# Optimization experiments

Hardware: AMD Instinct MI355X
Metric: run time of the kernel (lower is better)

## Reference

```python
import jax, jax.numpy as jnp
import numpy as np

B, C, H, W = 16, 512, 64, 64
G = 32
CG = C // G       # per-group channels = 16


def setup_inputs() -> dict:
    key = jax.random.key(0)
    ks = jax.random.split(key, 6)
    def w(k, shape, fan_in):
        return (jax.random.normal(k, shape, jnp.float32) / np.float32(np.sqrt(fan_in)))
    return {
        "x": jax.random.normal(ks[0], (B, C, H, W), jnp.float32),
        "conv1_w": w(ks[1], (CG, CG), CG), "conv1_b": jnp.zeros((CG,), jnp.float32),
        "convh_w": w(ks[2], (CG, CG), CG), "convh_b": jnp.zeros((CG,), jnp.float32),
        "convw_w": w(ks[3], (CG, CG), CG), "convw_b": jnp.zeros((CG,), jnp.float32),
        "conv3_w": w(ks[4], (CG, CG, 3, 3), CG * 9), "conv3_b": jnp.zeros((CG,), jnp.float32),
        "gn_w": jnp.ones((CG,), jnp.float32), "gn_b": jnp.zeros((CG,), jnp.float32),
    }


def _conv1x1(y, w, b):
    # y: [N, Ci, L]  w: [Co, Ci]  -> [N, Co, L]
    return jnp.einsum('oi,bil->bol', w, y) + b[None, :, None]


def _ema_forward(x, conv1_w, conv1_b, convh_w, convh_b, convw_w, convw_b,
                 conv3_w, conv3_b, gn_w, gn_b):
    b, c, h, w = x.shape
    g, cg, hw = G, CG, h * w
    bg = b * g
    xg = x.reshape(bg, cg, h, w)

    # coordinate pooling: row means [bg,cg,h], col means [bg,cg,w]
    x_h = xg.mean(axis=3)                     # [bg, cg, h]
    x_w = xg.mean(axis=2)                     # [bg, cg, w]
    y = jnp.concatenate([x_h, x_w], axis=2)   # [bg, cg, h+w]
    y = jax.nn.relu(_conv1x1(y, conv1_w, conv1_b))
    y_h, y_w = y[:, :, :h], y[:, :, h:]

    a_h = jax.nn.sigmoid(_conv1x1(y_h, convh_w, convh_b))[:, :, :, None]  # [bg,cg,h,1]
    a_w = jax.nn.sigmoid(_conv1x1(y_w, convw_w, convw_b))[:, :, None, :]  # [bg,cg,1,w]

    x1 = xg * a_h * a_w

    # GroupNorm(num_groups=1): normalize over (cg,h,w) per sample, affine per channel
    mu = x1.mean(axis=(1, 2, 3), keepdims=True)
    var = ((x1 - mu) ** 2).mean(axis=(1, 2, 3), keepdims=True)
    x2 = (x1 - mu) * jax.lax.rsqrt(var + 1e-5)
    x2 = x2 * gn_w[None, :, None, None] + gn_b[None, :, None, None]

    # 3x3 conv branch
    x3 = jax.lax.conv_general_dilated(
        xg, conv3_w, window_strides=(1, 1), padding='SAME',
        dimension_numbers=('NCHW', 'OIHW', 'NCHW'))
    x3 = jax.nn.relu(x3 + conv3_b[None, :, None, None])

    A2 = jax.nn.softmax(x2.reshape(bg, cg, hw), axis=-1)  # [bg,cg,hw]
    A3 = jax.nn.softmax(x3.reshape(bg, cg, hw), axis=-1)
    V2 = x2.mean(axis=(2, 3))                              # [bg,cg]
    V3 = x3.mean(axis=(2, 3))

    s2 = jnp.einsum('bc,bcl->bl', V2, A3)  # [bg, hw]
    s3 = jnp.einsum('bc,bcl->bl', V3, A2)
    s = jax.nn.softmax(s2 + s3, axis=-1).reshape(bg, 1, h, w)

    return (xg * s).reshape(b, c, h, w)


def reference(x, conv1_w, conv1_b, convh_w, convh_b, convw_w, convw_b,
              conv3_w, conv3_b, gn_w, gn_b):
    return _ema_forward(x, conv1_w, conv1_b, convh_w, convh_b, convw_w, convw_b,
                        conv3_w, conv3_b, gn_w, gn_b)
```

## Files before the change

### kernel.cpp

```cpp
#include <hip/hip_runtime.h>
#include <hip/hip_bf16.h>

#define CHW  65536
#define CHW4 16384

__device__ __forceinline__ float wred(float v){
#pragma unroll
  for (int o = 32; o; o >>= 1) v += __shfl_xor(v, o, 64);
  return v;
}
__device__ __forceinline__ float wred16(float v){
#pragma unroll
  for (int o = 8; o; o >>= 1) v += __shfl_xor(v, o, 64);
  return v;
}
__device__ __forceinline__ float bf2f(unsigned short u){
  return __uint_as_float(((unsigned)u) << 16);
}

__global__ __launch_bounds__(1024) void k1_attn(const float* __restrict__ x,
    const float* __restrict__ w1, const float* __restrict__ b1,
    const float* __restrict__ wh, const float* __restrict__ bh,
    const float* __restrict__ ww, const float* __restrict__ bw,
    float* __restrict__ aH, float* __restrict__ aW)
{
  __shared__ float rs[1024];
  __shared__ float cs[1024];
  __shared__ float ym[2048];
  int tid = threadIdx.x, bg = blockIdx.x;
  const float4* x4 = (const float4*)x + (size_t)bg * CHW4;
  cs[tid] = 0.f;
  __syncthreads();
  int h = tid >> 4, lane = tid & 63;
#pragma unroll 4
  for (int k = 0; k < 16; ++k){
    float4 v = x4[k*1024 + tid];
    float s = v.x + v.y + v.z + v.w;
    s = wred16(s);
    if ((tid & 15) == 0) rs[k*64 + h] = s;
    v.x += __shfl_xor(v.x, 16); v.x += __shfl_xor(v.x, 32);
    v.y += __shfl_xor(v.y, 16); v.y += __shfl_xor(v.y, 32);
    v.z += __shfl_xor(v.z, 16); v.z += __shfl_xor(v.z, 32);
    v.w += __shfl_xor(v.w, 16); v.w += __shfl_xor(v.w, 32);
    if (lane < 16){
      atomicAdd(&cs[k*64 + lane*4 + 0], v.x);
      atomicAdd(&cs[k*64 + lane*4 + 1], v.y);
      atomicAdd(&cs[k*64 + lane*4 + 2], v.z);
      atomicAdd(&cs[k*64 + lane*4 + 3], v.w);
    }
  }
  __syncthreads();
  for (int ol = tid; ol < 2048; ol += 1024){
    int o = ol >> 7, l = ol & 127;
    float acc = b1[o];
#pragma unroll
    for (int i = 0; i < 16; ++i){
      float mv = (l < 64 ? rs[i*64 + l] : cs[i*64 + (l-64)]) * (1.f/64.f);
      acc = fmaf(w1[o*16 + i], mv, acc);
    }
    ym[o*128 + l] = fmaxf(acc, 0.f);
  }
  __syncthreads();
  for (int ol = tid; ol < 2048; ol += 1024){
    int q = ol >> 10;
    int o = (ol >> 6) & 15;
    int p = ol & 63;
    const float* Wm = q ? ww : wh;
    float acc = q ? bw[o] : bh[o];
#pragma unroll
    for (int i = 0; i < 16; ++i)
      acc = fmaf(Wm[o*16 + i], ym[i*128 + q*64 + p], acc);
    float sg = 1.f / (1.f + __expf(-acc));
    (q ? aW : aH)[((size_t)bg*16 + o)*64 + p] = sg;
  }
}

__global__ __launch_bounds__(1024) void k2_stats(const float* __restrict__ x,
    const float* __restrict__ aH, const float* __restrict__ aW,
    const float* __restrict__ gnw, const float* __restrict__ gnb,
    float* __restrict__ MU, float* __restrict__ RSTD,
    float* __restrict__ V2, float* __restrict__ Z2)
{
  __shared__ __align__(16) float ahs[1024], aws[1024];
  __shared__ float chpart[256], zpart[256];
  __shared__ float red1[16], red2[16];
  __shared__ float murs[2], sc_s[16], of_s[16];
  int tid = threadIdx.x, bg = blockIdx.x;
  const float4* x4 = (const float4*)x + (size_t)bg * CHW4;
  ahs[tid] = aH[(size_t)bg*1024 + tid];
  aws[tid] = aW[(size_t)bg*1024 + tid];
  __syncthreads();
  int h = tid >> 4, w4 = tid & 15, lane = tid & 63, wv = tid >> 6;
  const float4* aws4 = (const float4*)aws;
  float s1 = 0.f, s2 = 0.f;
#pragma unroll 4
  for (int k = 0; k < 16; ++k){
    float4 v = x4[k*1024 + tid];
    float ah = ahs[k*64 + h];
    float4 aw = aws4[k*16 + w4];
    float4 x1;
    x1.x = v.x * ah * aw.x;
    x1.y = v.y * ah * aw.y;
    x1.z = v.z * ah * aw.z;
    x1.w = v.w * ah * aw.w;
    float csum = x1.x + x1.y + x1.z + x1.w;
    s1 += csum;
    s2 = fmaf(x1.x, x1.x, s2); s2 = fmaf(x1.y, x1.y, s2);
    s2 = fmaf(x1.z, x1.z, s2); s2 = fmaf(x1.w, x1.w, s2);
    float cw = wred(csum);
    if (lane == 0) chpart[k*16 + wv] = cw;
  }
  float r1 = wred(s1), r2 = wred(s2);
  if (lane == 0){ red1[wv] = r1; red2[wv] = r2; }
  __syncthreads();
  if (tid == 0){
    float S = 0.f, SS = 0.f;
#pragma unroll
    for (int i = 0; i < 16; ++i){ S += red1[i]; SS += red2[i]; }
    float mu = S * (1.f/65536.f);
    float var = SS * (1.f/65536.f) - mu*mu;
    float rstd = rsqrtf(var + 1e-5f);
    murs[0] = mu; murs[1] = rstd;
    MU[bg] = mu; RSTD[bg] = rstd;
  }
  __syncthreads();
  if (tid < 16){
    float ch = 0.f;
#pragma unroll
    for (int m = 0; m < 16; ++m) ch += chpart[tid*16 + m];
    float mu = murs[0], rstd = murs[1];
    float g = gnw[tid], b = gnb[tid];
    float sc = rstd * g;
    sc_s[tid] = sc; of_s[tid] = b - mu*sc;
    V2[(size_t)bg*16 + tid] = (ch * (1.f/4096.f) - mu) * sc + b;
  }
  __syncthreads();
#pragma unroll 2
  for (int k = 0; k < 16; ++k){
    float4 v = x4[k*1024 + tid];
    float ah = ahs[k*64 + h];
    float4 aw = aws4[k*16 + w4];
    float sc = sc_s[k], of = of_s[k];
    float z =  __expf(fmaf(v.x * ah * aw.x, sc, of));
    z += __expf(fmaf(v.y * ah * aw.y, sc, of));
    z += __expf(fmaf(v.z * ah * aw.z, sc, of));
    z += __expf(fmaf(v.w * ah * aw.w, sc, of));
    float zw = wred(z);
    if (lane == 0) zpart[k*16 + wv] = zw;
  }
  __syncthreads();
  if (tid < 16){
    float z = 0.f;
#pragma unroll
    for (int m = 0; m < 16; ++m) z += zpart[tid*16 + m];
    Z2[(size_t)bg*16 + tid] = z;
  }
}

#define STR 84
__global__ __launch_bounds__(256, 3) void k3_conv(const float* __restrict__ x,
    const float* __restrict__ w3, const float* __restrict__ b3,
    __hip_bfloat16* __restrict__ X3, float* __restrict__ V3, float* __restrict__ Z3)
{
  __shared__ __align__(16) float in_s[16*10*STR];
  int tid = threadIdx.x;
  int s   = blockIdx.x;
  int bg  = blockIdx.y;
  size_t base  = (size_t)bg * CHW;
  const float4* x4 = (const float4*)x + (size_t)bg * CHW4;
  int lane = tid & 63;
  int cog = __builtin_amdgcn_readfirstlane(tid >> 6);
  int co0 = cog * 4;
  int r  = lane >> 3;
  int w0 = (lane & 7) * 8;
  for (int idx = tid; idx < 2880; idx += 256){
    int q  = idx % 18;
    int rr = (idx / 18) % 10;
    int ci = idx / 180;
    int hh = s*8 - 1 + rr;
    float4 v = make_float4(0.f, 0.f, 0.f, 0.f);
    if (q >= 1 && q <= 16 && (unsigned)hh < 64u)
      v = x4[ci*1024 + hh*16 + (q-1)];
    *(float4*)&in_s[(ci*10 + rr)*STR + q*4] = v;
  }
  float bias[4];
#pragma unroll
  for (int i = 0; i < 4; ++i) bias[i] = b3[co0+i];
  float acc[4][8];
#pragma unroll
  for (int i = 0; i < 4; ++i)
#pragma unroll
    for (int px = 0; px < 8; ++px) acc[i][px] = 0.f;
  __syncthreads();
#pragma unroll 1
  for (int ci = 0; ci < 16; ++ci){
    float wgt[4][9];
#pragma unroll
    for (int i = 0; i < 4; ++i)
#pragma unroll
      for (int t = 0; t < 9; ++t)
        wgt[i][t] = w3[((co0+i)*16 + ci)*9 + t];
#pragma unroll
    for (int dy = 0; dy < 3; ++dy){
      const float* row = &in_s[(ci*10 + r + dy)*STR + w0];
      float4 A0 = *(const float4*)(row);
      float4 A1 = *(const float4*)(row+4);
      float4 A2v = *(const float4*)(row+8);
      float4 A3v = *(const float4*)(row+12);
      float v[16] = {A0.x,A0.y,A0.z,A0.w, A1.x,A1.y,A1.z,A1.w,
                     A2v.x,A2v.y,A2v.z,A2v.w, A3v.x,A3v.y,A3v.z,A3v.w};
#pragma unroll
      for (int dx = 0; dx < 3; ++dx){
#pragma unroll
        for (int px = 0; px < 8; ++px){
          float iv = v[px + dx + 3];
#pragma unroll
          for (int i = 0; i < 4; ++i)
            acc[i][px] = fmaf(wgt[i][dy*3+dx], iv, acc[i][px]);
        }
      }
    }
  }
  int hh = s*8 + r;
  float v3acc[4], z3acc[4];
#pragma unroll
  for (int i = 0; i < 4; ++i){
    union { __hip_bfloat16 hb[8]; uint4 u; } pk;
    v3acc[i] = 0.f; z3acc[i] = 0.f;
#pragma unroll
    for (int px = 0; px < 8; ++px){
      float val = fmaxf(acc[i][px] + bias[i], 0.f);
      __hip_bfloat16 hv = __float2bfloat16(val);
      float vq = __bfloat162float(hv);
      v3acc[i] += vq;
      z3acc[i] += __expf(vq);
      pk.hb[px] = hv;
    }
    *(uint4*)&X3[base + (size_t)(co0+i)*4096 + hh*64 + w0] = pk.u;
  }
#pragma unroll
  for (int i = 0; i < 4; ++i){
    float rv = wred(v3acc[i]);
    float rz = wred(z3acc[i]);
    if (lane == 0){
      atomicAdd(&V3[(size_t)bg*16 + co0 + i], rv);
      atomicAdd(&Z3[(size_t)bg*16 + co0 + i], rz);
    }
  }
}

__global__ __launch_bounds__(1024) void k4_final(const float* __restrict__ x,
    const __hip_bfloat16* __restrict__ X3,
    const float* __restrict__ aH, const float* __restrict__ aW,
    const float* __restrict__ gnw, const float* __restrict__ gnb,
    const float* __restrict__ MU, const float* __restrict__ RSTD,
    const float* __restrict__ V2, const float* __restrict__ Z2,
    const float* __restrict__ V3, const float* __restrict__ Z3,
    float* __restrict__ out)
{
  __shared__ __align__(16) float ahs[1024], aws[1024];
  __shared__ float sc_s[16], of_s[16], p2s[16], p3s[16], red[16];
  __shared__ float invS_s;
  int tid = threadIdx.x, bg = blockIdx.x;
  const float4* x4 = (const float4*)x + (size_t)bg * CHW4;
  const ushort4* X34 = (const ushort4*)X3 + (size_t)bg * CHW4;
  float4* o4 = (float4*)out + (size_t)bg * CHW4;
  ahs[tid] = aH[(size_t)bg*1024 + tid];
  aws[tid] = aW[(size_t)bg*1024 + tid];
  if (tid < 16){
    float mu = MU[bg], rstd = RSTD[bg];
    float g = gnw[tid], b = gnb[tid];
    float sc = rstd*g;
    sc_s[tid] = sc; of_s[tid] = b - mu*sc;
    p2s[tid] = V3[(size_t)bg*16+tid] * (1.f/4096.f) / Z2[(size_t)bg*16+tid];
    p3s[tid] = V2[(size_t)bg*16+tid] / Z3[(size_t)bg*16+tid];
  }
  __syncthreads();
  int h = tid >> 4, w4 = tid & 15, lane = tid & 63, wv = tid >> 6;
  const float4* aws4 = (const float4*)aws;
  float4 tacc = make_float4(0.f,0.f,0.f,0.f);
#pragma unroll 2
  for (int k = 0; k < 16; ++k){
    float4 v = x4[k*1024 + tid];
    ushort4 xu = X34[k*1024 + tid];
    float ah = ahs[k*64 + h];
    float4 aw = aws4[k*16 + w4];
    float sc = sc_s[k], of = of_s[k], p2 = p2s[k], p3 = p3s[k];
    tacc.x += __expf(fmaf(v.x*ah*aw.x, sc, of))*p2 + __expf(bf2f(xu.x))*p3;
    tacc.y += __expf(fmaf(v.y*ah*aw.y, sc, of))*p2 + __expf(bf2f(xu.y))*p3;
    tacc.z += __expf(fmaf(v.z*ah*aw.z, sc, of))*p2 + __expf(bf2f(xu.z))*p3;
    tacc.w += __expf(fmaf(v.w*ah*aw.w, sc, of))*p2 + __expf(bf2f(xu.w))*p3;
  }
  float4 e;
  e.x = __expf(tacc.x); e.y = __expf(tacc.y);
  e.z = __expf(tacc.z); e.w = __expf(tacc.w);
  float es = e.x + e.y + e.z + e.w;
  float r = wred(es);
  if (lane == 0) red[wv] = r;
  __syncthreads();
  if (tid == 0){
    float S = 0.f;
#pragma unroll
    for (int i = 0; i < 16; ++i) S += red[i];
    invS_s = 1.f / S;
  }
  __syncthreads();
  float iS = invS_s;
  float4 ei = make_float4(e.x*iS, e.y*iS, e.z*iS, e.w*iS);
#pragma unroll 4
  for (int k = 0; k < 16; ++k){
    float4 v = x4[k*1024 + tid];
    float4 ov;
    ov.x = v.x * ei.x; ov.y = v.y * ei.y;
    ov.z = v.z * ei.z; ov.w = v.w * ei.w;
    o4[k*1024 + tid] = ov;
  }
}

extern "C" void kernel_launch(void* const* d_in, const int* in_sizes, int n_in,
                              void* d_out, int out_size, void* d_ws, size_t ws_size,
                              hipStream_t stream)
{
  const float* x   = (const float*)d_in[0];
  const float* w1  = (const float*)d_in[1];
  const float* b1  = (const float*)d_in[2];
  const float* wh  = (const float*)d_in[3];
  const float* bh  = (const float*)d_in[4];
  const float* ww  = (const float*)d_in[5];
  const float* bw  = (const float*)d_in[6];
  const float* w3  = (const float*)d_in[7];
  const float* b3  = (const float*)d_in[8];
  const float* gnw = (const float*)d_in[9];
  const float* gnb = (const float*)d_in[10];
  float* out = (float*)d_out;

  float* Wp   = (float*)d_ws;
  float* aH   = Wp;
  float* aW_  = aH + 524288;
  float* MU   = aW_ + 524288;
  float* RSTD = MU + 512;
  float* V2   = RSTD + 512;
  float* Z2   = V2 + 8192;
  float* V3   = Z2 + 8192;
  float* Z3   = V3 + 8192;
  __hip_bfloat16* X3 = (__hip_bfloat16*)(Z3 + 8192);
  (void)ws_size; (void)n_in; (void)in_sizes; (void)out_size;

  hipMemsetAsync(V3, 0, 2 * 8192 * sizeof(float), stream);
  k1_attn <<<512, 1024, 0, stream>>>(x, w1, b1, wh, bh, ww, bw, aH, aW_);
  k3_conv <<<dim3(8, 512), 256, 0, stream>>>(x, w3, b3, X3, V3, Z3);
  k2_stats<<<512, 1024, 0, stream>>>(x, aH, aW_, gnw, gnb, MU, RSTD, V2, Z2);
  k4_final<<<512, 1024, 0, stream>>>(x, X3, aH, aW_, gnw, gnb, MU, RSTD, V2, Z2, V3, Z3, out);
}
```

Before: 512.6 us.

## Fuse attention, stats and final kernels into one megakernel; store exp of conv output

The attention, GroupNorm-stats and final softmax kernels are merged into a single per-group kernel that keeps the H/W attention vectors and statistics in shared memory instead of round-tripping through global memory. The conv kernel now stages input in two 8-channel halves to halve shared memory and raise occupancy. It stores exp(x3) in bf16 so the final pass skips one exp per element, and it writes per-strip partial sums instead of using atomics, which removes the memset. The risks are that the megakernel does three sequential passes over x within one block with heavy LDS use, and that bf16 rounding of exp values changes precision slightly.

```diff
diff --git a/kernel.cpp b/kernel.cpp
--- a/kernel.cpp
+++ b/kernel.cpp
@@ -18,26 +18,131 @@
   return __uint_as_float(((unsigned)u) << 16);
 }
 
-__global__ __launch_bounds__(1024) void k1_attn(const float* __restrict__ x,
+#define STR 84
+__global__ __launch_bounds__(256, 6) void k3_conv(const float* __restrict__ x,
+    const float* __restrict__ w3, const float* __restrict__ b3,
+    __hip_bfloat16* __restrict__ E3,
+    float* __restrict__ V3part, float* __restrict__ Z3part)
+{
+  __shared__ __align__(16) float in_s[8*10*STR];
+  int tid = threadIdx.x;
+  int s   = blockIdx.x;
+  int bg  = blockIdx.y;
+  size_t base  = (size_t)bg * CHW;
+  const float4* x4 = (const float4*)x + (size_t)bg * CHW4;
+  int lane = tid & 63;
+  int cog = __builtin_amdgcn_readfirstlane(tid >> 6);
+  int co0 = cog * 4;
+  int r  = lane >> 3;
+  int w0 = (lane & 7) * 8;
+  float acc[4][8];
+#pragma unroll
+  for (int i = 0; i < 4; ++i)
+#pragma unroll
+    for (int px = 0; px < 8; ++px) acc[i][px] = 0.f;
+
+#pragma unroll 1
+  for (int half = 0; half < 2; ++half){
+    __syncthreads();
+    for (int idx = tid; idx < 1440; idx += 256){
+      int q   = idx % 18;
+      int rr  = (idx / 18) % 10;
+      int ci8 = idx / 180;
+      int hh  = s*8 - 1 + rr;
+      float4 v = make_float4(0.f, 0.f, 0.f, 0.f);
+      if (q >= 1 && q <= 16 && (unsigned)hh < 64u)
+        v = x4[(half*8 + ci8)*1024 + hh*16 + (q-1)];
+      *(float4*)&in_s[(ci8*10 + rr)*STR + q*4] = v;
+    }
+    __syncthreads();
+#pragma unroll 1
+    for (int ci8 = 0; ci8 < 8; ++ci8){
+      int ci = half*8 + ci8;
+      float wgt[4][9];
+#pragma unroll
+      for (int i = 0; i < 4; ++i)
+#pragma unroll
+        for (int t = 0; t < 9; ++t)
+          wgt[i][t] = w3[((co0+i)*16 + ci)*9 + t];
+#pragma unroll
+      for (int dy = 0; dy < 3; ++dy){
+        const float* row = &in_s[(ci8*10 + r + dy)*STR + w0];
+        float4 A0 = *(const float4*)(row);
+        float4 A1 = *(const float4*)(row+4);
+        float4 A2v = *(const float4*)(row+8);
+        float4 A3v = *(const float4*)(row+12);
+        float v[16] = {A0.x,A0.y,A0.z,A0.w, A1.x,A1.y,A1.z,A1.w,
+                       A2v.x,A2v.y,A2v.z,A2v.w, A3v.x,A3v.y,A3v.z,A3v.w};
+#pragma unroll
+        for (int dx = 0; dx < 3; ++dx){
+#pragma unroll
+          for (int px = 0; px < 8; ++px){
+            float iv = v[px + dx + 3];
+#pragma unroll
+            for (int i = 0; i < 4; ++i)
+              acc[i][px] = fmaf(wgt[i][dy*3+dx], iv, acc[i][px]);
+          }
+        }
+      }
+    }
+  }
+  int hh = s*8 + r;
+#pragma unroll
+  for (int i = 0; i < 4; ++i){
+    float bias = b3[co0+i];
+    union { __hip_bfloat16 hb[8]; uint4 u; } pk;
+    float v3acc = 0.f, z3acc = 0.f;
+#pragma unroll
+    for (int px = 0; px < 8; ++px){
+      float val = fmaxf(acc[i][px] + bias, 0.f);
+      float e = __expf(val);
+      v3acc += val;
+      z3acc += e;
+      pk.hb[px] = __float2bfloat16(e);
+    }
+    *(uint4*)&E3[base + (size_t)(co0+i)*4096 + hh*64 + w0] = pk.u;
+    float rv = wred(v3acc);
+    float rz = wred(z3acc);
+    if (lane == 0){
+      V3part[((size_t)bg*8 + s)*16 + co0 + i] = rv;
+      Z3part[((size_t)bg*8 + s)*16 + co0 + i] = rz;
+    }
+  }
+}
+
+__global__ __launch_bounds__(1024, 8) void mega(const float* __restrict__ x,
     const float* __restrict__ w1, const float* __restrict__ b1,
     const float* __restrict__ wh, const float* __restrict__ bh,
     const float* __restrict__ ww, const float* __restrict__ bw,
-    float* __restrict__ aH, float* __restrict__ aW)
+    const float* __restrict__ gnw, const float* __restrict__ gnb,
+    const float* __restrict__ V3part, const float* __restrict__ Z3part,
+    const __hip_bfloat16* __restrict__ E3,
+    float* __restrict__ out)
 {
   __shared__ float rs[1024];
   __shared__ float cs[1024];
   __shared__ float ym[2048];
+  __shared__ __align__(16) float ahs[1024], aws[1024];
+  __shared__ float chpart[256], zpart[256];
+  __shared__ float red1[16], red2[16];
+  __shared__ float murs[2];
+  __shared__ float sc_s[16], of_s[16], v2_s[16], p2s[16], p3s[16];
+  __shared__ float invS_s;
+
   int tid = threadIdx.x, bg = blockIdx.x;
   const float4* x4 = (const float4*)x + (size_t)bg * CHW4;
+  const ushort4* E34 = (const ushort4*)E3 + (size_t)bg * CHW4;
+  float4* o4 = (float4*)out + (size_t)bg * CHW4;
+  int h = tid >> 4, w4 = tid & 15, lane = tid & 63, wv = tid >> 6;
+
   cs[tid] = 0.f;
   __syncthreads();
-  int h = tid >> 4, lane = tid & 63;
 #pragma unroll 4
   for (int k = 0; k < 16; ++k){
     float4 v = x4[k*1024 + tid];
-    float s = v.x + v.y + v.z + v.w;
-    s = wred16(s);
-    if ((tid & 15) == 0) rs[k*64 + h] = s;
+    float srow = v.x + v.y + v.z + v.w;
+    srow = wred16(srow);
+    if ((tid & 15) == 0) rs[k*64 + h] = srow;
     v.x += __shfl_xor(v.x, 16); v.x += __shfl_xor(v.x, 32);
     v.y += __shfl_xor(v.y, 16); v.y += __shfl_xor(v.y, 32);
     v.z += __shfl_xor(v.z, 16); v.z += __shfl_xor(v.z, 32);
@@ -71,26 +176,10 @@
     for (int i = 0; i < 16; ++i)
       acc = fmaf(Wm[o*16 + i], ym[i*128 + q*64 + p], acc);
     float sg = 1.f / (1.f + __expf(-acc));
-    (q ? aW : aH)[((size_t)bg*16 + o)*64 + p] = sg;
-  }
-}
-
-__global__ __launch_bounds__(1024) void k2_stats(const float* __restrict__ x,
-    const float* __restrict__ aH, const float* __restrict__ aW,
-    const float* __restrict__ gnw, const float* __restrict__ gnb,
-    float* __restrict__ MU, float* __restrict__ RSTD,
-    float* __restrict__ V2, float* __restrict__ Z2)
-{
-  __shared__ __align__(16) float ahs[1024], aws[1024];
-  __shared__ float chpart[256], zpart[256];
-  __shared__ float red1[16], red2[16];
-  __shared__ float murs[2], sc_s[16], of_s[16];
-  int tid = threadIdx.x, bg = blockIdx.x;
-  const float4* x4 = (const float4*)x + (size_t)bg * CHW4;
-  ahs[tid] = aH[(size_t)bg*1024 + tid];
-  aws[tid] = aW[(size_t)bg*1024 + tid];
-  __syncthreads();
-  int h = tid >> 4, w4 = tid & 15, lane = tid & 63, wv = tid >> 6;
+    (q ? aws : ahs)[o*64 + p] = sg;
+  }
+  __syncthreads();
+
   const float4* aws4 = (const float4*)aws;
   float s1 = 0.f, s2 = 0.f;
 #pragma unroll 4
@@ -119,9 +208,7 @@
     for (int i = 0; i < 16; ++i){ S += red1[i]; SS += red2[i]; }
     float mu = S * (1.f/65536.f);
     float var = SS * (1.f/65536.f) - mu*mu;
-    float rstd = rsqrtf(var + 1e-5f);
-    murs[0] = mu; murs[1] = rstd;
-    MU[bg] = mu; RSTD[bg] = rstd;
+    murs[0] = mu; murs[1] = rsqrtf(var + 1e-5f);
   }
   __syncthreads();
   if (tid < 16){
@@ -132,9 +219,10 @@
     float g = gnw[tid], b = gnb[tid];
     float sc = rstd * g;
     sc_s[tid] = sc; of_s[tid] = b - mu*sc;
-    V2[(size_t)bg*16 + tid] = (ch * (1.f/4096.f) - mu) * sc + b;
-  }
-  __syncthreads();
+    v2_s[tid] = (ch * (1.f/4096.f) - mu) * sc + b;
+  }
+  __syncthreads();
+
 #pragma unroll 2
   for (int k = 0; k < 16; ++k){
     float4 v = x4[k*1024 + tid];
@@ -150,163 +238,50 @@
   }
   __syncthreads();
   if (tid < 16){
-    float z = 0.f;
-#pragma unroll
-    for (int m = 0; m < 16; ++m) z += zpart[tid*16 + m];
-    Z2[(size_t)bg*16 + tid] = z;
-  }
-}
-
-#define STR 84
-__global__ __launch_bounds__(256, 3) void k3_conv(const float* __restrict__ x,
-    const float* __restrict__ w3, const float* __restrict__ b3,
-    __hip_bfloat16* __restrict__ X3, float* __restrict__ V3, float* __restrict__ Z3)
-{
-  __shared__ __align__(16) float in_s[16*10*STR];
-  int tid = threadIdx.x;
-  int s   = blockIdx.x;
-  int bg  = blockIdx.y;
-  size_t base  = (size_t)bg * CHW;
-  const float4* x4 = (const float4*)x + (size_t)bg * CHW4;
-  int lane = tid & 63;
-  int cog = __builtin_amdgcn_readfirstlane(tid >> 6);
-  int co0 = cog * 4;
-  int r  = lane >> 3;
-  int w0 = (lane & 7) * 8;
-  for (int idx = tid; idx < 2880; idx += 256){
-    int q  = idx % 18;
-    int rr = (idx / 18) % 10;
-    int ci = idx / 180;
-    int hh = s*8 - 1 + rr;
-    float4 v = make_float4(0.f, 0.f, 0.f, 0.f);
-    if (q >= 1 && q <= 16 && (unsigned)hh < 64u)
-      v = x4[ci*1024 + hh*16 + (q-1)];
-    *(float4*)&in_s[(ci*10 + rr)*STR + q*4] = v;
-  }
-  float bias[4];
-#pragma unroll
-  for (int i = 0; i < 4; ++i) bias[i] = b3[co0+i];
-  float acc[4][8];
-#pragma unroll
-  for (int i = 0; i < 4; ++i)
-#pragma unroll
-    for (int px = 0; px < 8; ++px) acc[i][px] = 0.f;
-  __syncthreads();
-#pragma unroll 1
-  for (int ci = 0; ci < 16; ++ci){
-    float wgt[4][9];
-#pragma unroll
-    for (int i = 0; i < 4; ++i)
-#pragma unroll
-      for (int t = 0; t < 9; ++t)
-        wgt[i][t] = w3[((co0+i)*16 + ci)*9 + t];
-#pragma unroll
-    for (int dy = 0; dy < 3; ++dy){
-      const float* row = &in_s[(ci*10 + r + dy)*STR + w0];
-      float4 A0 = *(const float4*)(row);
-      float4 A1 = *(const float4*)(row+4);
-      float4 A2v = *(const float4*)(row+8);
-      float4 A3v = *(const float4*)(row+12);
-      float v[16] = {A0.x,A0.y,A0.z,A0.w, A1.x,A1.y,A1.z,A1.w,
-                     A2v.x,A2v.y,A2v.z,A2v.w, A3v.x,A3v.y,A3v.z,A3v.w};
-#pragma unroll
-      for (int dx = 0; dx < 3; ++dx){
-#pragma unroll
-        for (int px = 0; px < 8; ++px){
-          float iv = v[px + dx + 3];
-#pragma unroll
-          for (int i = 0; i < 4; ++i)
-            acc[i][px] = fmaf(wgt[i][dy*3+dx], iv, acc[i][px]);
-        }
-      }
-    }
-  }
-  int hh = s*8 + r;
-  float v3acc[4], z3acc[4];
-#pragma unroll
-  for (int i = 0; i < 4; ++i){
-    union { __hip_bfloat16 hb[8]; uint4 u; } pk;
-    v3acc[i] = 0.f; z3acc[i] = 0.f;
-#pragma unroll
-    for (int px = 0; px < 8; ++px){
-      float val = fmaxf(acc[i][px] + bias[i], 0.f);
-      __hip_bfloat16 hv = __float2bfloat16(val);
-      float vq = __bfloat162float(hv);
-      v3acc[i] += vq;
-      z3acc[i] += __expf(vq);
-      pk.hb[px] = hv;
-    }
-    *(uint4*)&X3[base + (size_t)(co0+i)*4096 + hh*64 + w0] = pk.u;
-  }
-#pragma unroll
-  for (int i = 0; i < 4; ++i){
-    float rv = wred(v3acc[i]);
-    float rz = wred(z3acc[i]);
-    if (lane == 0){
-      atomicAdd(&V3[(size_t)bg*16 + co0 + i], rv);
-      atomicAdd(&Z3[(size_t)bg*16 + co0 + i], rz);
-    }
-  }
-}
-
-__global__ __launch_bounds__(1024) void k4_final(const float* __restrict__ x,
-    const __hip_bfloat16* __restrict__ X3,
-    const float* __restrict__ aH, const float* __restrict__ aW,
-    const float* __restrict__ gnw, const float* __restrict__ gnb,
-    const float* __restrict__ MU, const float* __restrict__ RSTD,
-    const float* __restrict__ V2, const float* __restrict__ Z2,
-    const float* __restrict__ V3, const float* __restrict__ Z3,
-    float* __restrict__ out)
-{
-  __shared__ __align__(16) float ahs[1024], aws[1024];
-  __shared__ float sc_s[16], of_s[16], p2s[16], p3s[16], red[16];
-  __shared__ float invS_s;
-  int tid = threadIdx.x, bg = blockIdx.x;
-  const float4* x4 = (const float4*)x + (size_t)bg * CHW4;
-  const ushort4* X34 = (const ushort4*)X3 + (size_t)bg * CHW4;
-  float4* o4 = (float4*)out + (size_t)bg * CHW4;
-  ahs[tid] = aH[(size_t)bg*1024 + tid];
-  aws[tid] = aW[(size_t)bg*1024 + tid];
-  if (tid < 16){
-    float mu = MU[bg], rstd = RSTD[bg];
-    float g = gnw[tid], b = gnb[tid];
-    float sc = rstd*g;
-    sc_s[tid] = sc; of_s[tid] = b - mu*sc;
-    p2s[tid] = V3[(size_t)bg*16+tid] * (1.f/4096.f) / Z2[(size_t)bg*16+tid];
-    p3s[tid] = V2[(size_t)bg*16+tid] / Z3[(size_t)bg*16+tid];
-  }
-  __syncthreads();
-  int h = tid >> 4, w4 = tid & 15, lane = tid & 63, wv = tid >> 6;
-  const float4* aws4 = (const float4*)aws;
+    float z2 = 0.f;
+#pragma unroll
+    for (int m = 0; m < 16; ++m) z2 += zpart[tid*16 + m];
+    float v3 = 0.f, z3 = 0.f;
+#pragma unroll
+    for (int ss = 0; ss < 8; ++ss){
+      v3 += V3part[((size_t)bg*8 + ss)*16 + tid];
+      z3 += Z3part[((size_t)bg*8 + ss)*16 + tid];
+    }
+    p2s[tid] = v3 * (1.f/4096.f) / z2;
+    p3s[tid] = v2_s[tid] / z3;
+  }
+  __syncthreads();
+
   float4 tacc = make_float4(0.f,0.f,0.f,0.f);
 #pragma unroll 2
   for (int k = 0; k < 16; ++k){
     float4 v = x4[k*1024 + tid];
-    ushort4 xu = X34[k*1024 + tid];
+    ushort4 eu = E34[k*1024 + tid];
     float ah = ahs[k*64 + h];
     float4 aw = aws4[k*16 + w4];
     float sc = sc_s[k], of = of_s[k], p2 = p2s[k], p3 = p3s[k];
-    tacc.x += __expf(fmaf(v.x*ah*aw.x, sc, of))*p2 + __expf(bf2f(xu.x))*p3;
-    tacc.y += __expf(fmaf(v.y*ah*aw.y, sc, of))*p2 + __expf(bf2f(xu.y))*p3;
-    tacc.z += __expf(fmaf(v.z*ah*aw.z, sc, of))*p2 + __expf(bf2f(xu.z))*p3;
-    tacc.w += __expf(fmaf(v.w*ah*aw.w, sc, of))*p2 + __expf(bf2f(xu.w))*p3;
+    tacc.x += __expf(fmaf(v.x*ah*aw.x, sc, of))*p2 + bf2f(eu.x)*p3;
+    tacc.y += __expf(fmaf(v.y*ah*aw.y, sc, of))*p2 + bf2f(eu.y)*p3;
+    tacc.z += __expf(fmaf(v.z*ah*aw.z, sc, of))*p2 + bf2f(eu.z)*p3;
+    tacc.w += __expf(fmaf(v.w*ah*aw.w, sc, of))*p2 + bf2f(eu.w)*p3;
   }
   float4 e;
   e.x = __expf(tacc.x); e.y = __expf(tacc.y);
   e.z = __expf(tacc.z); e.w = __expf(tacc.w);
   float es = e.x + e.y + e.z + e.w;
-  float r = wred(es);
-  if (lane == 0) red[wv] = r;
+  float rr = wred(es);
+  if (lane == 0) red1[wv] = rr;
   __syncthreads();
   if (tid == 0){
     float S = 0.f;
 #pragma unroll
-    for (int i = 0; i < 16; ++i) S += red[i];
+    for (int i = 0; i < 16; ++i) S += red1[i];
     invS_s = 1.f / S;
   }
   __syncthreads();
   float iS = invS_s;
   float4 ei = make_float4(e.x*iS, e.y*iS, e.z*iS, e.w*iS);
+
 #pragma unroll 4
   for (int k = 0; k < 16; ++k){
     float4 v = x4[k*1024 + tid];
@@ -334,21 +309,12 @@
   const float* gnb = (const float*)d_in[10];
   float* out = (float*)d_out;
 
-  float* Wp   = (float*)d_ws;
-  float* aH   = Wp;
-  float* aW_  = aH + 524288;
-  float* MU   = aW_ + 524288;
-  float* RSTD = MU + 512;
-  float* V2   = RSTD + 512;
-  float* Z2   = V2 + 8192;
-  float* V3   = Z2 + 8192;
-  float* Z3   = V3 + 8192;
-  __hip_bfloat16* X3 = (__hip_bfloat16*)(Z3 + 8192);
+  float* V3part = (float*)d_ws;
+  float* Z3part = V3part + 65536;
+  __hip_bfloat16* E3 = (__hip_bfloat16*)(Z3part + 65536);
   (void)ws_size; (void)n_in; (void)in_sizes; (void)out_size;
 
-  hipMemsetAsync(V3, 0, 2 * 8192 * sizeof(float), stream);
-  k1_attn <<<512, 1024, 0, stream>>>(x, w1, b1, wh, bh, ww, bw, aH, aW_);
-  k3_conv <<<dim3(8, 512), 256, 0, stream>>>(x, w3, b3, X3, V3, Z3);
-  k2_stats<<<512, 1024, 0, stream>>>(x, aH, aW_, gnw, gnb, MU, RSTD, V2, Z2);
-  k4_final<<<512, 1024, 0, stream>>>(x, X3, aH, aW_, gnw, gnb, MU, RSTD, V2, Z2, V3, Z3, out);
-}
+  k3_conv<<<dim3(8, 512), 256, 0, stream>>>(x, w3, b3, E3, V3part, Z3part);
+  mega   <<<512, 1024, 0, stream>>>(x, w1, b1, wh, bh, ww, bw, gnw, gnb,
+                                    V3part, Z3part, E3, out);
+}
```

New measurement: 476.8 us. 1.08x faster.
